# Kernel tuning notes

Hardware: AMD Instinct MI355X
Metric: run time of the kernel (lower is better)

The kernel has to match this reference:

```python
import jax, jax.numpy as jnp
import numpy as np
import math

D_MODEL = 1024
N_HEADS = 16
HEAD_DIM = D_MODEL // N_HEADS
B, T = 4, 2048


def setup_inputs() -> dict:
    key = jax.random.key(0)
    k1, k2, k3, k4, k5 = jax.random.split(key, 5)
    s = 1.0 / math.sqrt(D_MODEL)
    return {
        "x": jax.random.normal(k1, (B, T, D_MODEL), dtype=jnp.float32),
        "qkv_w": jax.random.normal(k2, (3 * D_MODEL, D_MODEL), dtype=jnp.float32) * s,
        "qkv_b": jax.random.normal(k3, (3 * D_MODEL,), dtype=jnp.float32) * 0.02,
        "out_w": jax.random.normal(k4, (D_MODEL, D_MODEL), dtype=jnp.float32) * s,
        "out_b": jax.random.normal(k5, (D_MODEL,), dtype=jnp.float32) * 0.02,
    }


def reference(x, qkv_w, qkv_b, out_w, out_b) -> jnp.ndarray:
    b, t, c = x.shape
    h, hd = N_HEADS, HEAD_DIM
    # qkv projection: [B,T,3C]
    qkv = jnp.einsum("btc,oc->bto", x, qkv_w) + qkv_b
    qkv = qkv.reshape(b, t, 3, h, hd).transpose(2, 0, 3, 1, 4)  # [3,B,H,T,hd]
    q, k, v = qkv[0], qkv[1], qkv[2]
    scale = 1.0 / math.sqrt(hd)
    attn = jnp.einsum("bhqd,bhkd->bhqk", q, k) * scale  # [B,H,T,T]
    causal = jnp.triu(jnp.ones((t, t), dtype=bool), k=1)
    attn = jnp.where(causal, -jnp.inf, attn)
    attn = jax.nn.softmax(attn, axis=-1)
    out = jnp.einsum("bhqk,bhkd->bhqd", attn, v)  # [B,H,T,hd]
    out = out.transpose(0, 2, 1, 3).reshape(b, t, c)
    return jnp.einsum("btc,oc->bto", out, out_w) + out_b
```

## Files before the change

### kernel.cpp

```cpp
#include <hip/hip_runtime.h>
#include <stdint.h>
#include <stddef.h>

#define TT 2048
#define NH 16
#define HD 64
#define CM 1024
#define QSCALE 0.1803368801f
#define PPAD 72

typedef float f32x4  __attribute__((ext_vector_type(4)));
typedef short bf16x8 __attribute__((ext_vector_type(8)));

static __device__ __forceinline__ unsigned short f32_to_bf16(float f) {
    union { float f; unsigned u; } c; c.f = f;
    unsigned u = c.u;
    u += 0x7FFFu + ((u >> 16) & 1u);
    return (unsigned short)(u >> 16);
}

static __device__ __forceinline__ unsigned pack_bf16_trunc(float lo, float hi) {
    return __builtin_amdgcn_perm(__float_as_uint(hi), __float_as_uint(lo), 0x07060302u);
}

static __device__ __forceinline__ void glds16(const unsigned short* g, unsigned short* l) {
    __builtin_amdgcn_global_load_lds(
        (const __attribute__((address_space(1))) unsigned int*)g,
        (__attribute__((address_space(3))) unsigned int*)l,
        16, 0, 0);
}

static __device__ __forceinline__ void hard_barrier() {
    asm volatile("s_waitcnt vmcnt(0) lgkmcnt(0)" ::: "memory");
    __syncthreads();
}

__global__ __launch_bounds__(256) void cast_all(
    const float* __restrict__ x, const float* __restrict__ w1,
    const float* __restrict__ w2,
    unsigned short* __restrict__ X16, unsigned short* __restrict__ W1o,
    unsigned short* __restrict__ W2o) {
    int i = blockIdx.x * blockDim.x + threadIdx.x;
    const float* src; unsigned short* dst; int j;
    if (i < 2097152)      { src = x;  dst = X16; j = i; }
    else if (i < 2883584) { src = w1; dst = W1o; j = i - 2097152; }
    else                  { src = w2; dst = W2o; j = i - 2883584; }
    float4 v = ((const float4*)src)[j];
    ushort4 o;
    o.x = f32_to_bf16(v.x); o.y = f32_to_bf16(v.y);
    o.z = f32_to_bf16(v.z); o.w = f32_to_bf16(v.w);
    ((ushort4*)dst)[j] = o;
}

template<bool SWAP>
__device__ __forceinline__ void gemm256_core(
    const unsigned short* __restrict__ A,
    const unsigned short* __restrict__ Bm,
    int m0, int n0,
    unsigned short* lds,
    f32x4 acc[8][4])
{
    const int tid  = threadIdx.x;
    const int lane = tid & 63;
    const int w    = tid >> 6;
    const int l15  = lane & 15;
    const int quad = lane >> 4;
    const int wm   = (w >> 1) * 128;
    const int wn   = (w & 1) * 64;
    const int ro   = (quad ^ (l15 & 3)) * 8;

    const int rr = tid >> 2;
    const int ch = (tid & 3) ^ (rr & 3);
    const unsigned short* gA = A  + (size_t)(m0 + rr) * CM + ch * 8;
    const unsigned short* gB = Bm + (size_t)(n0 + rr) * CM + ch * 8;
    const int wb = (tid & ~63) * 8;

    unsigned short* ldsA = lds;
    unsigned short* ldsB = lds + 16384;

#define STAGE6(bb)                                                    \
    {                                                                 \
        unsigned short* dA = ldsA + (bb) * 8192 + wb;                 \
        unsigned short* dB = ldsB + (bb) * 4096 + wb;                 \
        glds16(gA,            dA);                                    \
        glds16(gA +  64 * CM, dA + 2048);                             \
        glds16(gA + 128 * CM, dA + 4096);                             \
        glds16(gA + 192 * CM, dA + 6144);                             \
        glds16(gB,            dB);                                    \
        glds16(gB +  64 * CM, dB + 2048);                             \
        gA += 32; gB += 32;                                           \
    }

    STAGE6(0);
    STAGE6(1);

    for (int t = 0; t < 32; ++t) {
        if (t > 0) {
            asm volatile("s_waitcnt lgkmcnt(0)" ::: "memory");
            __builtin_amdgcn_s_barrier();
            asm volatile("" ::: "memory");
            if (t + 1 < 32) STAGE6((t + 1) & 1);
        }
        if (t + 1 < 32) asm volatile("s_waitcnt vmcnt(6)" ::: "memory");
        else            asm volatile("s_waitcnt vmcnt(0)" ::: "memory");
        __builtin_amdgcn_s_barrier();
        asm volatile("" ::: "memory");

        const unsigned short* tA = ldsA + (t & 1) * 8192;
        const unsigned short* tB = ldsB + (t & 1) * 4096;

        bf16x8 bfr[4];
        #pragma unroll
        for (int ni = 0; ni < 4; ++ni)
            bfr[ni] = *(const bf16x8*)(tB + (wn + ni * 16 + l15) * 32 + ro);
        bf16x8 af[8];
        #pragma unroll
        for (int mi = 0; mi < 8; ++mi)
            af[mi] = *(const bf16x8*)(tA + (wm + mi * 16 + l15) * 32 + ro);

        #pragma unroll
        for (int mi = 0; mi < 8; ++mi)
            #pragma unroll
            for (int ni = 0; ni < 4; ++ni)
                acc[mi][ni] = SWAP
                    ? __builtin_amdgcn_mfma_f32_16x16x32_bf16(bfr[ni], af[mi], acc[mi][ni], 0, 0, 0)
                    : __builtin_amdgcn_mfma_f32_16x16x32_bf16(af[mi], bfr[ni], acc[mi][ni], 0, 0, 0);
    }
#undef STAGE6
}

__global__ __launch_bounds__(256, 2) void gemm_qkv(
    const unsigned short* __restrict__ X,
    const unsigned short* __restrict__ W,
    const float* __restrict__ bias,
    unsigned short* __restrict__ Qb,
    unsigned short* __restrict__ Kb,
    unsigned short* __restrict__ Vt)
{
    __shared__ __align__(16) unsigned short lds[24576];
    const int m0 = blockIdx.y * 256;
    const int n0 = blockIdx.x * 128;

    f32x4 acc[8][4];
    f32x4 z = {0.f, 0.f, 0.f, 0.f};
    #pragma unroll
    for (int mi = 0; mi < 8; ++mi)
        #pragma unroll
        for (int ni = 0; ni < 4; ++ni) acc[mi][ni] = z;

    const int region = n0 >> 10;
    if (region < 2) gemm256_core<true >(X, W, m0, n0, lds, acc);
    else            gemm256_core<false>(X, W, m0, n0, lds, acc);

    const int tid  = threadIdx.x;
    const int lane = tid & 63;
    const int w    = tid >> 6;
    const int wm   = (w >> 1) * 128;
    const int wn   = (w & 1) * 64;
    const int l15  = lane & 15;
    const int quad = lane >> 4;
    const int b_idx = m0 >> 11;
    const int t0 = m0 & 2047;

    if (region == 2) {
        hard_barrier();
        #pragma unroll
        for (int hn = 0; hn < 2; ++hn) {
            if ((w & 1) == hn) {
                #pragma unroll
                for (int ni = 0; ni < 4; ++ni) {
                    const int nloc = ni * 16 + l15;
                    const float bv = bias[n0 + hn * 64 + nloc];
                    #pragma unroll
                    for (int mi = 0; mi < 8; ++mi) {
                        uint2 pk;
                        pk.x = (unsigned)f32_to_bf16(acc[mi][ni][0] + bv) |
                               ((unsigned)f32_to_bf16(acc[mi][ni][1] + bv) << 16);
                        pk.y = (unsigned)f32_to_bf16(acc[mi][ni][2] + bv) |
                               ((unsigned)f32_to_bf16(acc[mi][ni][3] + bv) << 16);
                        *(uint2*)(lds + nloc * 264 + wm + mi * 16 + quad * 4) = pk;
                    }
                }
            }
            hard_barrier();
            {
                const int row = tid >> 2, seg = tid & 3;
                const int o   = n0 + hn * 64 + row;
                const int oin = o & 1023;
                const int hh  = oin >> 6, d = oin & 63;
                unsigned short* dst = Vt + ((size_t)((b_idx << 4) + hh) * HD + d) * TT
                                        + t0 + seg * 64;
                const unsigned short* src = lds + row * 264 + seg * 64;
                #pragma unroll
                for (int u = 0; u < 8; ++u)
                    *(uint4*)(dst + u * 8) = *(const uint4*)(src + u * 8);
            }
            hard_barrier();
        }
        return;
    }

    unsigned short* dst0 = region ? Kb : Qb;
    const float scl = region ? 1.0f : QSCALE;
    #pragma unroll
    for (int mi = 0; mi < 8; ++mi) {
        const int gm = m0 + wm + mi * 16 + l15;
        const int t  = gm & 2047;
        #pragma unroll
        for (int ni = 0; ni < 4; ++ni) {
            const int o  = n0 + wn + ni * 16 + quad * 4;
            const float4 bv = *(const float4*)(bias + o);
            const int oin = o & 1023;
            const int hh = oin >> 6, d = oin & 63;
            const int bh = (b_idx << 4) + hh;
            const float v0 = (acc[mi][ni][0] + bv.x) * scl;
            const float v1 = (acc[mi][ni][1] + bv.y) * scl;
            const float v2 = (acc[mi][ni][2] + bv.z) * scl;
            const float v3 = (acc[mi][ni][3] + bv.w) * scl;
            uint2 pk;
            pk.x = (unsigned)f32_to_bf16(v0) | ((unsigned)f32_to_bf16(v1) << 16);
            pk.y = (unsigned)f32_to_bf16(v2) | ((unsigned)f32_to_bf16(v3) << 16);
            *(uint2*)(dst0 + (((size_t)(bh * TT + t)) << 6) + d) = pk;
        }
    }
}

__global__ __launch_bounds__(256, 2) void attn_kernel(
    const unsigned short* __restrict__ Qb,
    const unsigned short* __restrict__ Kb,
    const unsigned short* __restrict__ Vt,
    unsigned short* __restrict__ CTX)
{
    __shared__ __align__(16) unsigned short Kl[3][4096];
    __shared__ __align__(16) unsigned short Vl[3][4096];
    __shared__ __align__(16) unsigned short Pl[4][16 * PPAD];

    const int id = blockIdx.x;
    const int qt = 15 - (id >> 6);
    const int bh = id & 63;
    const int b  = bh >> 4, h = bh & 15;
    const int tid  = threadIdx.x;
    const int lane = tid & 63;
    const int w    = tid >> 6;
    const int l15  = lane & 15;
    const int quad = lane >> 4;
    const int sw   = l15 & 7;
    const int bhh  = b * NH + h;

    const unsigned short* Kbase = Kb + (size_t)bhh * TT * HD;
    const unsigned short* Vbase = Vt + (size_t)bhh * HD * TT;
    const f32x4 z = {0.f, 0.f, 0.f, 0.f};

    const int c1 = tid, c2 = tid + 256;
    const int row1 = c1 >> 3, col1 = ((c1 & 7) ^ (row1 & 7)) * 8;
    const int row2 = c2 >> 3, col2 = ((c2 & 7) ^ (row2 & 7)) * 8;
    unsigned short* dK1 = &Kl[0][(c1 & ~63) * 8];
    unsigned short* dK2 = &Kl[0][(c2 & ~63) * 8];
    unsigned short* dV1 = &Vl[0][(c1 & ~63) * 8];
    unsigned short* dV2 = &Vl[0][(c2 & ~63) * 8];

    const int len = 2 * qt + 2;
    const int qb0 = qt * 128;

    const unsigned short* kp1 = Kbase + (size_t)row1 * HD + col1;
    const unsigned short* kp2 = Kbase + (size_t)row2 * HD + col2;
    const unsigned short* vp1 = Vbase + (size_t)row1 * TT + col1;
    const unsigned short* vp2 = Vbase + (size_t)row2 * TT + col2;

    bf16x8 qf[2][2];
    #pragma unroll
    for (int f = 0; f < 2; ++f) {
        const unsigned short* qr =
            Qb + (size_t)(bhh * TT + qb0 + f * 64 + w * 16 + l15) * HD + quad * 8;
        qf[f][0] = *(const bf16x8*)(qr);
        qf[f][1] = *(const bf16x8*)(qr + 32);
    }

    f32x4 o_acc[2][4];
    #pragma unroll
    for (int f = 0; f < 2; ++f)
        #pragma unroll
        for (int di = 0; di < 4; ++di) o_acc[f][di] = z;
    float lrun[2] = {0.f, 0.f};

#define STAGE_KV(bufidx)                                               \
    {                                                                  \
        const int nx = (bufidx) * 4096;                                \
        glds16(kp1, dK1 + nx); glds16(kp2, dK2 + nx);                  \
        glds16(vp1, dV1 + nx); glds16(vp2, dV2 + nx);                  \
        kp1 += 64 * HD; kp2 += 64 * HD; vp1 += 64; vp2 += 64;          \
    }
    STAGE_KV(0);
    STAGE_KV(1);
    if (len > 2) STAGE_KV(2);

    for (int i = 0; i < len; ++i) {
        const int cur = i % 3;
        if (i > 0) {
            asm volatile("s_waitcnt lgkmcnt(0)" ::: "memory");
            __builtin_amdgcn_s_barrier();
            asm volatile("" ::: "memory");
            if (i + 2 < len) STAGE_KV((i + 2) % 3);
        }
        if (i + 2 < len)      asm volatile("s_waitcnt vmcnt(8)" ::: "memory");
        else if (i + 1 < len) asm volatile("s_waitcnt vmcnt(4)" ::: "memory");
        else                  asm volatile("s_waitcnt vmcnt(0)" ::: "memory");
        __builtin_amdgcn_s_barrier();
        asm volatile("" ::: "memory");

        const unsigned short* Kt    = &Kl[0][0] + cur * 4096;
        const unsigned short* Vtile = &Vl[0][0] + cur * 4096;
        const bool f0act = (i < len - 1);

        f32x4 s0[4], s1[4];
        __builtin_amdgcn_s_setprio(1);
        #pragma unroll
        for (int ni = 0; ni < 4; ++ni) {
            const unsigned short* kr = Kt + (ni * 16 + l15) * 64;
            bf16x8 kf0 = *(const bf16x8*)(kr + ((quad ^ sw) * 8));
            bf16x8 kf1 = *(const bf16x8*)(kr + (((quad + 4) ^ sw) * 8));
            if (f0act) {
                f32x4 a = __builtin_amdgcn_mfma_f32_16x16x32_bf16(kf0, qf[0][0], z, 0, 0, 0);
                s0[ni] = __builtin_amdgcn_mfma_f32_16x16x32_bf16(kf1, qf[0][1], a, 0, 0, 0);
            }
            f32x4 a1 = __builtin_amdgcn_mfma_f32_16x16x32_bf16(kf0, qf[1][0], z, 0, 0, 0);
            s1[ni] = __builtin_amdgcn_mfma_f32_16x16x32_bf16(kf1, qf[1][1], a1, 0, 0, 0);
        }
        __builtin_amdgcn_s_setprio(0);

        const int qloc = w * 16 + l15;
        if (f0act && i == len - 2) {
            #pragma unroll
            for (int ni = 0; ni < 4; ++ni)
                #pragma unroll
                for (int r = 0; r < 4; ++r)
                    if (ni * 16 + quad * 4 + r > qloc) s0[ni][r] = -1e30f;
        }
        if (i == len - 1) {
            #pragma unroll
            for (int ni = 0; ni < 4; ++ni)
                #pragma unroll
                for (int r = 0; r < 4; ++r)
                    if (ni * 16 + quad * 4 + r > qloc) s1[ni][r] = -1e30f;
        }

        #define SOFTMAX_P(S, F)                                              \
        {                                                                    \
            float tni[4];                                                    \
            _Pragma("unroll")                                                \
            for (int ni = 0; ni < 4; ++ni) {                                 \
                float p0 = __builtin_amdgcn_exp2f(S[ni][0]);                 \
                float p1 = __builtin_amdgcn_exp2f(S[ni][1]);                 \
                float p2 = __builtin_amdgcn_exp2f(S[ni][2]);                 \
                float p3 = __builtin_amdgcn_exp2f(S[ni][3]);                 \
                S[ni][0] = p0; S[ni][1] = p1; S[ni][2] = p2; S[ni][3] = p3;  \
                tni[ni] = (p0 + p1) + (p2 + p3);                             \
            }                                                                \
            lrun[F] += (tni[0] + tni[1]) + (tni[2] + tni[3]);                \
            unsigned short* pwf = Pl[w];                                     \
            _Pragma("unroll")                                                \
            for (int ni = 0; ni < 4; ++ni) {                                 \
                uint2 pk;                                                    \
                pk.x = pack_bf16_trunc(S[ni][0], S[ni][1]);                  \
                pk.y = pack_bf16_trunc(S[ni][2], S[ni][3]);                  \
                *(uint2*)(pwf + l15 * PPAD + ni * 16 + quad * 4) = pk;       \
            }                                                                \
        }

        bf16x8 vf[2][4];
        SOFTMAX_P(s1, 1);
        asm volatile("s_waitcnt lgkmcnt(0)" ::: "memory");
        __builtin_amdgcn_s_setprio(1);
        #pragma unroll
        for (int c = 0; c < 2; ++c) {
            bf16x8 pf1 = *(const bf16x8*)(Pl[w] + l15 * PPAD + c * 32 + quad * 8);
            #pragma unroll
            for (int di = 0; di < 4; ++di) {
                vf[c][di] = *(const bf16x8*)(Vtile + (di * 16 + l15) * 64
                                           + (((c * 4 + quad) ^ sw) * 8));
                o_acc[1][di] = __builtin_amdgcn_mfma_f32_16x16x32_bf16(vf[c][di], pf1, o_acc[1][di], 0, 0, 0);
            }
        }
        __builtin_amdgcn_s_setprio(0);
        if (f0act) {
            SOFTMAX_P(s0, 0);
            asm volatile("s_waitcnt lgkmcnt(0)" ::: "memory");
            __builtin_amdgcn_s_setprio(1);
            #pragma unroll
            for (int c = 0; c < 2; ++c) {
                bf16x8 pf0 = *(const bf16x8*)(Pl[w] + l15 * PPAD + c * 32 + quad * 8);
                #pragma unroll
                for (int di = 0; di < 4; ++di)
                    o_acc[0][di] = __builtin_amdgcn_mfma_f32_16x16x32_bf16(vf[c][di], pf0, o_acc[0][di], 0, 0, 0);
            }
            __builtin_amdgcn_s_setprio(0);
        }
        #undef SOFTMAX_P
    }
#undef STAGE_KV

    #pragma unroll
    for (int f = 0; f < 2; ++f) {
        float lt = lrun[f];
        lt += __shfl_xor(lt, 16);
        lt += __shfl_xor(lt, 32);
        const float inv = 1.0f / lt;
        unsigned short* crow =
            CTX + (size_t)(b * TT + qb0 + f * 64 + w * 16 + l15) * CM + h * HD;
        #pragma unroll
        for (int di = 0; di < 4; ++di) {
            uint2 pk;
            pk.x = (unsigned)f32_to_bf16(o_acc[f][di][0] * inv) |
                   ((unsigned)f32_to_bf16(o_acc[f][di][1] * inv) << 16);
            pk.y = (unsigned)f32_to_bf16(o_acc[f][di][2] * inv) |
                   ((unsigned)f32_to_bf16(o_acc[f][di][3] * inv) << 16);
            *(uint2*)(crow + di * 16 + quad * 4) = pk;
        }
    }
}

__global__ __launch_bounds__(256, 2) void gemm_out(
    const unsigned short* __restrict__ CTX,
    const unsigned short* __restrict__ W,
    const float* __restrict__ bias,
    float* __restrict__ out)
{
    __shared__ __align__(16) unsigned short lds[24576];
    const int m0 = blockIdx.y * 256;
    const int n0 = blockIdx.x * 128;

    f32x4 acc[8][4];
    f32x4 z = {0.f, 0.f, 0.f, 0.f};
    #pragma unroll
    for (int mi = 0; mi < 8; ++mi)
        #pragma unroll
        for (int ni = 0; ni < 4; ++ni) acc[mi][ni] = z;

    gemm256_core<true>(CTX, W, m0, n0, lds, acc);

    const int tid  = threadIdx.x;
    const int lane = tid & 63;
    const int w    = tid >> 6;
    const int wm   = (w >> 1) * 128;
    const int wn   = (w & 1) * 64;
    const int l15  = lane & 15;
    const int quad = lane >> 4;

    #pragma unroll
    for (int mi = 0; mi < 8; ++mi) {
        const int gm = m0 + wm + mi * 16 + l15;
        float* orow = out + (size_t)gm * CM;
        #pragma unroll
        for (int ni = 0; ni < 4; ++ni) {
            const int o = n0 + wn + ni * 16 + quad * 4;
            const float4 bv = *(const float4*)(bias + o);
            float4 v;
            v.x = acc[mi][ni][0] + bv.x;
            v.y = acc[mi][ni][1] + bv.y;
            v.z = acc[mi][ni][2] + bv.z;
            v.w = acc[mi][ni][3] + bv.w;
            *(float4*)(orow + o) = v;
        }
    }
}

extern "C" void kernel_launch(void* const* d_in, const int* in_sizes, int n_in,
                              void* d_out, int out_size, void* d_ws, size_t ws_size,
                              hipStream_t stream) {
    const float* x     = (const float*)d_in[0];
    const float* qkv_w = (const float*)d_in[1];
    const float* qkv_b = (const float*)d_in[2];
    const float* out_w = (const float*)d_in[3];
    const float* out_b = (const float*)d_in[4];
    float* out = (float*)d_out;

    char* ws = (char*)d_ws;
    unsigned short* X16 = (unsigned short*)(ws + 0);
    unsigned short* W1  = (unsigned short*)(ws + 16777216);
    unsigned short* W2  = (unsigned short*)(ws + 23068672);
    unsigned short* Qb  = (unsigned short*)(ws + 25165824);
    unsigned short* Kb  = (unsigned short*)(ws + 41943040);
    unsigned short* Vt  = (unsigned short*)(ws + 58720256);
    unsigned short* CTX = (unsigned short*)(ws + 75497472);

    cast_all<<<12288, 256, 0, stream>>>(x, qkv_w, out_w, X16, W1, W2);

    gemm_qkv<<<dim3(24, 32), 256, 0, stream>>>(X16, W1, qkv_b, Qb, Kb, Vt);
    attn_kernel<<<1024, 256, 0, stream>>>(Qb, Kb, Vt, CTX);
    gemm_out<<<dim3(8, 32), 256, 0, stream>>>(CTX, W2, out_b, out);
}
```

Measured before the change: 254.4 us.

## Use 256x256 tiles with 8 waves and split-phase pipelined mainloop in QKV GEMM

Replaces the 256x128, 4-wave QKV projection GEMM with a 256x256 tile run by 512 threads (8 waves). The new loop uses a 4-deep LDS ring buffer with direct global-to-LDS loads and splits each k-step into two half-phases, interleaving half of the next-tile loads with each MFMA batch. It also raises wave priority during MFMA bursts. The aim is better operand reuse, halving the grid, and overlapping memory with compute. The cost is 128KB of LDS per block and heavy register pressure, which may limit occupancy to one block per CU. The V-transpose epilogue is reworked to match the new wave layout.

```diff
diff --git a/kernel.cpp b/kernel.cpp
--- a/kernel.cpp
+++ b/kernel.cpp
@@ -129,7 +129,108 @@
 #undef STAGE6
 }
 
-__global__ __launch_bounds__(256, 2) void gemm_qkv(
+template<bool SWAP>
+__device__ __forceinline__ void gemm8p_core(
+    const unsigned short* __restrict__ A,
+    const unsigned short* __restrict__ Bm,
+    int m0, int n0,
+    unsigned short* lds,
+    f32x4 acc[8][4])
+{
+    const int tid  = threadIdx.x;
+    const int lane = tid & 63;
+    const int w    = tid >> 6;
+    const int l15  = lane & 15;
+    const int quad = lane >> 4;
+    const int wm   = (w >> 2) * 128;
+    const int wn   = (w & 3) * 64;
+    const int ro   = (quad ^ (l15 & 3)) * 8;
+
+    unsigned short* ldsA = lds;
+    unsigned short* ldsB = lds + 32768;
+
+    const int c1 = tid, c2 = tid + 512;
+    const int r1 = c1 >> 2, s1 = ((c1 & 3) ^ (r1 & 3)) * 8;
+    const int r2 = c2 >> 2, s2 = ((c2 & 3) ^ (r2 & 3)) * 8;
+    const unsigned short* gA1 = A  + (size_t)(m0 + r1) * CM + s1;
+    const unsigned short* gA2 = A  + (size_t)(m0 + r2) * CM + s2;
+    const unsigned short* gB1 = Bm + (size_t)(n0 + r1) * CM + s1;
+    const unsigned short* gB2 = Bm + (size_t)(n0 + r2) * CM + s2;
+    unsigned short* dA1 = ldsA + (c1 & ~63) * 8;
+    unsigned short* dA2 = ldsA + (c2 & ~63) * 8;
+    unsigned short* dB1 = ldsB + (c1 & ~63) * 8;
+    unsigned short* dB2 = ldsB + (c2 & ~63) * 8;
+
+#define STAGE_H8(T, half)                                             \
+    {                                                                 \
+        const int bo = ((T) & 3) * 8192;                              \
+        const int ko = (T) * 32;                                      \
+        if ((half) == 0) {                                            \
+            glds16(gA1 + ko, dA1 + bo);                               \
+            glds16(gB1 + ko, dB1 + bo);                               \
+        } else {                                                      \
+            glds16(gA2 + ko, dA2 + bo);                               \
+            glds16(gB2 + ko, dB2 + bo);                               \
+        }                                                             \
+    }
+#define STAGE_T8(T) { STAGE_H8(T, 0); STAGE_H8(T, 1); }
+
+    STAGE_T8(0); STAGE_T8(1); STAGE_T8(2);
+
+    for (int T = 0; T < 32; ++T) {
+        if (T <= 29)      asm volatile("s_waitcnt vmcnt(8)" ::: "memory");
+        else if (T == 30) asm volatile("s_waitcnt vmcnt(4)" ::: "memory");
+        else              asm volatile("s_waitcnt vmcnt(0)" ::: "memory");
+        __builtin_amdgcn_s_barrier();
+        asm volatile("" ::: "memory");
+
+        const unsigned short* tA = ldsA + (T & 3) * 8192;
+        const unsigned short* tB = ldsB + (T & 3) * 8192;
+
+        if (T + 3 < 32) STAGE_H8(T + 3, 0);
+        bf16x8 bfr[4], af[4];
+        #pragma unroll
+        for (int ni = 0; ni < 4; ++ni)
+            bfr[ni] = *(const bf16x8*)(tB + (wn + ni * 16 + l15) * 32 + ro);
+        #pragma unroll
+        for (int mi = 0; mi < 4; ++mi)
+            af[mi] = *(const bf16x8*)(tA + (wm + mi * 16 + l15) * 32 + ro);
+        asm volatile("s_waitcnt lgkmcnt(0)" ::: "memory");
+        __builtin_amdgcn_s_setprio(1);
+        #pragma unroll
+        for (int mi = 0; mi < 4; ++mi)
+            #pragma unroll
+            for (int ni = 0; ni < 4; ++ni)
+                acc[mi][ni] = SWAP
+                    ? __builtin_amdgcn_mfma_f32_16x16x32_bf16(bfr[ni], af[mi], acc[mi][ni], 0, 0, 0)
+                    : __builtin_amdgcn_mfma_f32_16x16x32_bf16(af[mi], bfr[ni], acc[mi][ni], 0, 0, 0);
+        __builtin_amdgcn_s_setprio(0);
+        __builtin_amdgcn_s_barrier();
+        asm volatile("" ::: "memory");
+
+        if (T + 3 < 32) STAGE_H8(T + 3, 1);
+        bf16x8 af2[4];
+        #pragma unroll
+        for (int mi = 0; mi < 4; ++mi)
+            af2[mi] = *(const bf16x8*)(tA + (wm + 64 + mi * 16 + l15) * 32 + ro);
+        asm volatile("s_waitcnt lgkmcnt(0)" ::: "memory");
+        __builtin_amdgcn_s_setprio(1);
+        #pragma unroll
+        for (int mi = 0; mi < 4; ++mi)
+            #pragma unroll
+            for (int ni = 0; ni < 4; ++ni)
+                acc[4 + mi][ni] = SWAP
+                    ? __builtin_amdgcn_mfma_f32_16x16x32_bf16(bfr[ni], af2[mi], acc[4 + mi][ni], 0, 0, 0)
+                    : __builtin_amdgcn_mfma_f32_16x16x32_bf16(af2[mi], bfr[ni], acc[4 + mi][ni], 0, 0, 0);
+        __builtin_amdgcn_s_setprio(0);
+        __builtin_amdgcn_s_barrier();
+        asm volatile("" ::: "memory");
+    }
+#undef STAGE_T8
+#undef STAGE_H8
+}
+
+__global__ __launch_bounds__(512, 2) void gemm_qkv(
     const unsigned short* __restrict__ X,
     const unsigned short* __restrict__ W,
     const float* __restrict__ bias,
@@ -137,9 +238,9 @@
     unsigned short* __restrict__ Kb,
     unsigned short* __restrict__ Vt)
 {
-    __shared__ __align__(16) unsigned short lds[24576];
+    __shared__ __align__(16) unsigned short lds[65536];
     const int m0 = blockIdx.y * 256;
-    const int n0 = blockIdx.x * 128;
+    const int n0 = blockIdx.x * 256;
 
     f32x4 acc[8][4];
     f32x4 z = {0.f, 0.f, 0.f, 0.f};
@@ -149,14 +250,14 @@
         for (int ni = 0; ni < 4; ++ni) acc[mi][ni] = z;
 
     const int region = n0 >> 10;
-    if (region < 2) gemm256_core<true >(X, W, m0, n0, lds, acc);
-    else            gemm256_core<false>(X, W, m0, n0, lds, acc);
+    if (region < 2) gemm8p_core<true >(X, W, m0, n0, lds, acc);
+    else            gemm8p_core<false>(X, W, m0, n0, lds, acc);
 
     const int tid  = threadIdx.x;
     const int lane = tid & 63;
     const int w    = tid >> 6;
-    const int wm   = (w >> 1) * 128;
-    const int wn   = (w & 1) * 64;
+    const int wm   = (w >> 2) * 128;
+    const int wn   = (w & 3) * 64;
     const int l15  = lane & 15;
     const int quad = lane >> 4;
     const int b_idx = m0 >> 11;
@@ -165,12 +266,12 @@
     if (region == 2) {
         hard_barrier();
         #pragma unroll
-        for (int hn = 0; hn < 2; ++hn) {
-            if ((w & 1) == hn) {
+        for (int half = 0; half < 2; ++half) {
+            if ((w >> 2) == half) {
                 #pragma unroll
                 for (int ni = 0; ni < 4; ++ni) {
-                    const int nloc = ni * 16 + l15;
-                    const float bv = bias[n0 + hn * 64 + nloc];
+                    const int nloc = wn + ni * 16 + l15;
+                    const float bv = bias[n0 + nloc];
                     #pragma unroll
                     for (int mi = 0; mi < 8; ++mi) {
                         uint2 pk;
@@ -178,19 +279,18 @@
                                ((unsigned)f32_to_bf16(acc[mi][ni][1] + bv) << 16);
                         pk.y = (unsigned)f32_to_bf16(acc[mi][ni][2] + bv) |
                                ((unsigned)f32_to_bf16(acc[mi][ni][3] + bv) << 16);
-                        *(uint2*)(lds + nloc * 264 + wm + mi * 16 + quad * 4) = pk;
+                        *(uint2*)(lds + nloc * 132 + mi * 16 + quad * 4) = pk;
                     }
                 }
             }
             hard_barrier();
             {
-                const int row = tid >> 2, seg = tid & 3;
-                const int o   = n0 + hn * 64 + row;
-                const int oin = o & 1023;
+                const int row = tid >> 1, seg = tid & 1;
+                const int oin = (n0 & 1023) + row;
                 const int hh  = oin >> 6, d = oin & 63;
                 unsigned short* dst = Vt + ((size_t)((b_idx << 4) + hh) * HD + d) * TT
-                                        + t0 + seg * 64;
-                const unsigned short* src = lds + row * 264 + seg * 64;
+                                        + t0 + half * 128 + seg * 64;
+                const unsigned short* src = lds + row * 132 + seg * 64;
                 #pragma unroll
                 for (int u = 0; u < 8; ++u)
                     *(uint4*)(dst + u * 8) = *(const uint4*)(src + u * 8);
@@ -485,7 +585,7 @@
 
     cast_all<<<12288, 256, 0, stream>>>(x, qkv_w, out_w, X16, W1, W2);
 
-    gemm_qkv<<<dim3(24, 32), 256, 0, stream>>>(X16, W1, qkv_b, Qb, Kb, Vt);
+    gemm_qkv<<<dim3(12, 32), 512, 0, stream>>>(X16, W1, qkv_b, Qb, Kb, Vt);
     attn_kernel<<<1024, 256, 0, stream>>>(Qb, Kb, Vt, CTX);
     gemm_out<<<dim3(8, 32), 256, 0, stream>>>(CTX, W2, out_b, out);
 }
```

After: 270.9 us. +6.5%, slower.
